# Performance work log

Measured on AMD Instinct MI355X. Metric: run time of the kernel, lower is better.

## Reference

```python
import jax, jax.numpy as jnp
import numpy as np

N_EMBD = 768
N_HEAD = 12
B, T = 4, 2048
EPS = 1e-5


def layernorm(x, w, b):
    mu = jnp.mean(x, axis=-1, keepdims=True)
    var = jnp.mean(jnp.square(x - mu), axis=-1, keepdims=True)
    return (x - mu) * jax.lax.rsqrt(var + EPS) * w + b


def setup_inputs() -> dict:
    key = jax.random.key(0)
    ks = jax.random.split(key, 6)
    C = N_EMBD
    s = 0.02
    return {
        "x": jax.random.normal(ks[0], (B, T, C), jnp.float32),
        "ln1_w": jnp.ones((C,), jnp.float32),
        "ln1_b": jnp.zeros((C,), jnp.float32),
        "W_qkv": jax.random.normal(ks[1], (C, 3 * C), jnp.float32) * s,
        "b_qkv": jnp.zeros((3 * C,), jnp.float32),
        "W_attnproj": jax.random.normal(ks[2], (C, C), jnp.float32) * s,
        "b_attnproj": jnp.zeros((C,), jnp.float32),
        "ln2_w": jnp.ones((C,), jnp.float32),
        "ln2_b": jnp.zeros((C,), jnp.float32),
        "W_fc": jax.random.normal(ks[3], (C, 4 * C), jnp.float32) * s,
        "b_fc": jnp.zeros((4 * C,), jnp.float32),
        "W_mlpproj": jax.random.normal(ks[4], (4 * C, C), jnp.float32) * s,
        "b_mlpproj": jnp.zeros((C,), jnp.float32),
    }


def reference(x, ln1_w, ln1_b, W_qkv, b_qkv, W_attnproj, b_attnproj,
              ln2_w, ln2_b, W_fc, b_fc, W_mlpproj, b_mlpproj):
    Bx, Tx, C = x.shape
    H = N_HEAD
    Dh = C // H

    # --- attention branch ---
    h = layernorm(x, ln1_w, ln1_b)
    qkv = h @ W_qkv + b_qkv                       # [B, T, 3C]
    q, k, v = jnp.split(qkv, 3, axis=-1)
    q = q.reshape(Bx, Tx, H, Dh).transpose(0, 2, 1, 3)  # [B, H, T, Dh]
    k = k.reshape(Bx, Tx, H, Dh).transpose(0, 2, 1, 3)
    v = v.reshape(Bx, Tx, H, Dh).transpose(0, 2, 1, 3)
    att = jnp.einsum('bhqd,bhkd->bhqk', q, k) * (1.0 / np.sqrt(Dh))
    att = jax.nn.softmax(att, axis=-1)            # full softmax attention (no mask)
    y = jnp.einsum('bhqk,bhkd->bhqd', att, v)     # [B, H, T, Dh]
    y = y.transpose(0, 2, 1, 3).reshape(Bx, Tx, C)
    y = y @ W_attnproj + b_attnproj
    x = x + y

    # --- MLP branch ---
    h = layernorm(x, ln2_w, ln2_b)
    h = jax.nn.gelu(h @ W_fc + b_fc, approximate=False)
    h = h @ W_mlpproj + b_mlpproj
    return x + h
```

## Files before the change

### kernel.cpp

```cpp
#include <hip/hip_runtime.h>

typedef __bf16 bf16x8 __attribute__((ext_vector_type(8)));
typedef __bf16 bf16x4 __attribute__((ext_vector_type(4)));
typedef float f32x4 __attribute__((ext_vector_type(4)));
typedef unsigned short u16;
typedef unsigned long long u64;

#define GL2LDS(gp, lp) __builtin_amdgcn_global_load_lds(                      \
    (const __attribute__((address_space(1))) void*)(gp),                      \
    (__attribute__((address_space(3))) void*)(lp), 16, 0, 0)

__device__ __forceinline__ u16 f2u(float f) {
    __bf16 h = (__bf16)f;
    return __builtin_bit_cast(u16, h);
}

__device__ __forceinline__ float fexp2(float x) {
    float r;
    asm("v_exp_f32 %0, %1" : "=v"(r) : "v"(x));
    return r;
}

__device__ __forceinline__ float frcp(float x) {
    float r;
    asm("v_rcp_f32 %0, %1" : "=v"(r) : "v"(x));
    return r;
}

__device__ __forceinline__ float gelu(float x) {
    const float a = x * x;
    const float b = fmaf(a, 0.10294323f, 2.30220795f);
    const float u = fexp2(x * b);
    const float r = frcp(1.0f + u);
    return (x > 8.0f) ? x : x * u * r;
}

template <int N>
__device__ __forceinline__ void waitv() {
    if constexpr (N == 0) asm volatile("s_waitcnt vmcnt(0)" ::: "memory");
    else if constexpr (N == 3) asm volatile("s_waitcnt vmcnt(3)" ::: "memory");
    else if constexpr (N == 4) asm volatile("s_waitcnt vmcnt(4)" ::: "memory");
    else if constexpr (N == 6) asm volatile("s_waitcnt vmcnt(6)" ::: "memory");
    else if constexpr (N == 8) asm volatile("s_waitcnt vmcnt(8)" ::: "memory");
}

__device__ __forceinline__ f32x4 mfma16(bf16x8 a, bf16x8 b, f32x4 c) {
    return __builtin_amdgcn_mfma_f32_16x16x32_bf16(a, b, c, 0, 0, 0);
}

__global__ __launch_bounds__(256) void transpose_kernel(
    const float* __restrict__ W, u16* __restrict__ Wt, int K, int N) {
    __shared__ float tile[32][33];
    const int tx = threadIdx.x & 31, ty = threadIdx.x >> 5;
    const int n0 = blockIdx.x * 32, k0 = blockIdx.y * 32;
#pragma unroll
    for (int i = 0; i < 4; i++)
        tile[ty + 8 * i][tx] = W[(size_t)(k0 + ty + 8 * i) * N + n0 + tx];
    __syncthreads();
#pragma unroll
    for (int i = 0; i < 4; i++)
        Wt[(size_t)(n0 + ty + 8 * i) * K + k0 + tx] = f2u(tile[tx][ty + 8 * i]);
}

__global__ __launch_bounds__(256) void ln_kernel(
    const float* __restrict__ xin, const float* __restrict__ wgt,
    const float* __restrict__ bia, u16* __restrict__ outp) {
    const int row = blockIdx.x, t = threadIdx.x;
    const float* xr = xin + (size_t)row * 768;
    float v0 = xr[t], v1 = xr[t + 256], v2 = xr[t + 512];
    float s = v0 + v1 + v2;
    float ss = v0 * v0 + v1 * v1 + v2 * v2;
#pragma unroll
    for (int off = 32; off; off >>= 1) {
        s += __shfl_xor(s, off);
        ss += __shfl_xor(ss, off);
    }
    __shared__ float red[8];
    const int w = t >> 6;
    if ((t & 63) == 0) { red[w] = s; red[4 + w] = ss; }
    __syncthreads();
    s  = red[0] + red[1] + red[2] + red[3];
    ss = red[4] + red[5] + red[6] + red[7];
    const float mu = s * (1.f / 768.f);
    const float var = ss * (1.f / 768.f) - mu * mu;
    const float rs = rsqrtf(var + 1e-5f);
    u16* orow = outp + (size_t)row * 768;
    orow[t]       = f2u((v0 - mu) * rs * wgt[t]       + bia[t]);
    orow[t + 256] = f2u((v1 - mu) * rs * wgt[t + 256] + bia[t + 256]);
    orow[t + 512] = f2u((v2 - mu) * rs * wgt[t + 512] + bia[t + 512]);
}

template <int BM, int BN, int DEPTH, int EPI>
__global__ __launch_bounds__(256, 3) void gemm_bt(
    const u16* __restrict__ A, const u16* __restrict__ Bt,
    const float* __restrict__ bias, const float* __restrict__ res,
    void* __restrict__ outp, u16* __restrict__ vt, int M, int N, int K) {
    constexpr int MM = BM / 32;
    constexpr int NN = BN / 32;
    constexpr int L = BM / 64 + BN / 64;
    constexpr int NBUF = DEPTH + 1;
    __shared__ __align__(16) u16 As[NBUF][BM * 32];
    __shared__ __align__(16) u16 Bs[NBUF][BN * 32];
    const int t = threadIdx.x;
    const int lane = t & 63, w = t >> 6;
    const int wg0 = blockIdx.y * gridDim.x + blockIdx.x;
    const int xcd = wg0 & 7, loc = wg0 >> 3;
    const int gx = gridDim.x, gy = gridDim.y;
    const int m0 = (xcd * (gy >> 3) + loc / gx) * BM;
    const int n0 = (loc % gx) * BN;
    const int wm = (w >> 1) * (BM / 2), wn = (w & 1) * (BN / 2);
    const int lq = lane & 15, g = lane >> 4;

    f32x4 acc[MM][NN];
#pragma unroll
    for (int i = 0; i < MM; i++)
#pragma unroll
        for (int j = 0; j < NN; j++) acc[i][j] = (f32x4){0.f, 0.f, 0.f, 0.f};

    const int srow = t >> 2;
    const int scl = (t & 3) ^ ((t >> 3) & 3);
    const u16* gA0 = A + (size_t)(m0 + srow) * K + scl * 8;
    const u16* gA1 = A + (size_t)(m0 + 64 + srow) * K + scl * 8;
    const u16* gB0 = Bt + (size_t)(n0 + srow) * K + scl * 8;
    const u16* gB1 = Bt + (size_t)(n0 + 64 + srow) * K + scl * 8;

    const int cph = g ^ ((lq >> 1) & 3);
    const int KT = K >> 5;

#define STAGE(buf, kt)                                                        \
    do {                                                                      \
        const int k0_ = (kt) << 5;                                            \
        char* lA_ = (char*)As[buf] + w * 1024;                                \
        char* lB_ = (char*)Bs[buf] + w * 1024;                                \
        GL2LDS(gA0 + k0_, lA_);                                               \
        if (BM == 128) GL2LDS(gA1 + k0_, lA_ + 4096);                         \
        GL2LDS(gB0 + k0_, lB_);                                               \
        if (BN == 128) GL2LDS(gB1 + k0_, lB_ + 4096);                         \
    } while (0)

#pragma unroll
    for (int d = 0; d < DEPTH; d++) STAGE(d, d);
    int cur = 0;
    for (int kt = 0; kt < KT; ++kt) {
        const int ahead = KT - 1 - kt;
        if (ahead >= DEPTH - 1) waitv<(DEPTH - 1) * L>();
        else if (DEPTH == 3 && ahead == 1) waitv<L>();
        else waitv<0>();
        __builtin_amdgcn_s_barrier();
        __builtin_amdgcn_sched_barrier(0);
        const char* rA = (char*)As[cur] + (wm + lq) * 64 + cph * 16;
        const char* rB = (char*)Bs[cur] + (wn + lq) * 64 + cph * 16;
        bf16x8 af[MM], bfr[NN];
#pragma unroll
        for (int m = 0; m < MM; m++) af[m] = *(const bf16x8*)(rA + m * 1024);
#pragma unroll
        for (int n = 0; n < NN; n++) bfr[n] = *(const bf16x8*)(rB + n * 1024);
#pragma unroll
        for (int m = 0; m < MM; m++)
#pragma unroll
            for (int n = 0; n < NN; n++)
                acc[m][n] = mfma16(af[m], bfr[n], acc[m][n]);
        if (kt + DEPTH < KT) {
            int nb = cur + DEPTH;
            if (nb >= NBUF) nb -= NBUF;
            STAGE(nb, kt + DEPTH);
        }
        cur = (cur == NBUF - 1) ? 0 : cur + 1;
    }
#undef STAGE

#pragma unroll
    for (int n = 0; n < NN; n++) {
        const int col = n0 + wn + 16 * n + lq;
        const float bv = bias[col];
#pragma unroll
        for (int m = 0; m < MM; m++) {
            const int rbase = m0 + wm + 16 * m + 4 * g;
            if constexpr (EPI == 0) {
                if (col < 1536) {
                    const float sc = (col < 768) ? 0.18033688f : 1.0f;
#pragma unroll
                    for (int r = 0; r < 4; r++) {
                        const size_t idx = (size_t)(rbase + r) * N + col;
                        ((u16*)outp)[idx] = f2u((acc[m][n][r] + bv) * sc);
                    }
                } else {
                    const int d = col - 1536;
                    bf16x4 pk;
#pragma unroll
                    for (int r = 0; r < 4; r++)
                        pk[r] = (__bf16)(acc[m][n][r] + bv);
                    u16* vrow = vt +
                        ((size_t)((rbase >> 11) * 12 + (d >> 6)) * 64 + (d & 63)) * 2048 +
                        (rbase & 2047);
                    *(u64*)vrow = __builtin_bit_cast(u64, pk);
                }
            } else {
#pragma unroll
                for (int r = 0; r < 4; r++) {
                    const size_t idx = (size_t)(rbase + r) * N + col;
                    const float v = acc[m][n][r] + bv;
                    if constexpr (EPI == 1) {
                        ((float*)outp)[idx] = v + res[idx];
                    } else {
                        ((u16*)outp)[idx] = f2u(gelu(v));
                    }
                }
            }
        }
    }
}

__global__ __launch_bounds__(256, 3) void attn_kernel(
    const u16* __restrict__ qkv, const u16* __restrict__ Vt,
    u16* __restrict__ y) {
    __shared__ __align__(16) u16 Ks[2][4096];
    __shared__ __align__(16) u16 Vts[2][4096];
    __shared__ __align__(16) u16 Ps[4][2048];
    const int t = threadIdx.x, lane = t & 63, w = t >> 6;
    int wg = blockIdx.y * gridDim.x + blockIdx.x;
    wg = (wg & 7) * ((gridDim.x * gridDim.y) >> 3) + (wg >> 3);
    const int bh = wg / gridDim.x;
    const int b = bh / 12, h = bh % 12;
    const int q0 = (wg % gridDim.x) * 128 + w * 32;
    const int lq = lane & 15, g = lane >> 4;
    const int swz = (lq & 7) << 4;

    bf16x8 qf[2][2];
#pragma unroll
    for (int qh = 0; qh < 2; qh++) {
        const u16* qp =
            qkv + (size_t)(b * 2048 + q0 + qh * 16 + lq) * 2304 + h * 64 + g * 8;
        qf[qh][0] = *(const bf16x8*)(qp);
        qf[qh][1] = *(const bf16x8*)(qp + 32);
    }
    bf16x8 ones;
#pragma unroll
    for (int i = 0; i < 8; i++) ones[i] = (__bf16)1.0f;

    f32x4 acc_o[2][4], acc_s[2];
#pragma unroll
    for (int qh = 0; qh < 2; qh++) {
        acc_s[qh] = (f32x4){0.f, 0.f, 0.f, 0.f};
#pragma unroll
        for (int f = 0; f < 4; f++) acc_o[qh][f] = (f32x4){0.f, 0.f, 0.f, 0.f};
    }

    const int srow = t >> 3, sc = (t & 7) ^ (srow & 7);
    const u16* kg = qkv + 768 + h * 64 + sc * 8 + (size_t)(b * 2048 + srow) * 2304;
    const u16* vg = Vt + (size_t)(bh * 64 + srow) * 2048 + sc * 8;

    int cur = 0;
    GL2LDS(kg, (char*)Ks[0] + w * 1024);
    GL2LDS(kg + (size_t)32 * 2304, (char*)Ks[0] + w * 1024 + 4096);
    GL2LDS(vg, (char*)Vts[0] + w * 1024);
    GL2LDS(vg + 32 * 2048, (char*)Vts[0] + w * 1024 + 4096);
    __syncthreads();

    for (int k0 = 0; k0 < 2048; k0 += 64) {
        if (k0 + 64 < 2048) {
            const int kn = k0 + 64;
            GL2LDS(kg + (size_t)kn * 2304, (char*)Ks[cur ^ 1] + w * 1024);
            GL2LDS(kg + (size_t)(kn + 32) * 2304,
                   (char*)Ks[cur ^ 1] + w * 1024 + 4096);
            GL2LDS(vg + kn, (char*)Vts[cur ^ 1] + w * 1024);
            GL2LDS(vg + 32 * 2048 + kn, (char*)Vts[cur ^ 1] + w * 1024 + 4096);
        }
        const char* KB = (const char*)Ks[cur];
        const char* VB = (const char*)Vts[cur];

        f32x4 st[2][4];
        __builtin_amdgcn_s_setprio(1);
#pragma unroll
        for (int kb = 0; kb < 4; kb++) {
            st[0][kb] = (f32x4){0.f, 0.f, 0.f, 0.f};
            st[1][kb] = (f32x4){0.f, 0.f, 0.f, 0.f};
            const char* kr = KB + (kb * 16 + lq) * 128;
#pragma unroll
            for (int dh = 0; dh < 2; dh++) {
                const bf16x8 kf =
                    *(const bf16x8*)(kr + ((((dh << 2) + g) << 4) ^ swz));
                st[0][kb] = mfma16(kf, qf[0][dh], st[0][kb]);
                st[1][kb] = mfma16(kf, qf[1][dh], st[1][kb]);
            }
        }
        __builtin_amdgcn_s_setprio(0);

#pragma unroll
        for (int qh = 0; qh < 2; qh++) {
            char* pw = (char*)Ps[w] + (qh * 16 + lq) * 128 + ((g & 1) << 3);
#pragma unroll
            for (int kb = 0; kb < 4; kb++) {
                bf16x4 pb;
#pragma unroll
                for (int r = 0; r < 4; r++)
                    pb[r] = (__bf16)fexp2(st[qh][kb][r]);
                *(u64*)(pw + ((((kb << 1) + (g >> 1)) << 4) ^ swz)) =
                    __builtin_bit_cast(u64, pb);
            }
        }

        __builtin_amdgcn_s_setprio(1);
#pragma unroll
        for (int kk = 0; kk < 2; kk++) {
            const int co = ((kk << 2) + g) << 4;
            bf16x8 vf[4];
#pragma unroll
            for (int f = 0; f < 4; f++)
                vf[f] = *(const bf16x8*)(VB + (16 * f + lq) * 128 + (co ^ swz));
#pragma unroll
            for (int qh = 0; qh < 2; qh++) {
                const bf16x8 pf = *(const bf16x8*)(
                    (const char*)Ps[w] + (qh * 16 + lq) * 128 + (co ^ swz));
#pragma unroll
                for (int f = 0; f < 4; f++)
                    acc_o[qh][f] = mfma16(vf[f], pf, acc_o[qh][f]);
                acc_s[qh] = mfma16(ones, pf, acc_s[qh]);
            }
        }
        __builtin_amdgcn_s_setprio(0);
        __syncthreads();
        cur ^= 1;
    }

#pragma unroll
    for (int qh = 0; qh < 2; qh++) {
        const float rinv = frcp(acc_s[qh][0]);
        char* yb = (char*)(y + (size_t)(b * 2048 + q0 + qh * 16 + lq) * 768 +
                           h * 64);
#pragma unroll
        for (int f = 0; f < 4; f++) {
            bf16x4 pk;
#pragma unroll
            for (int r = 0; r < 4; r++) pk[r] = (__bf16)(acc_o[qh][f][r] * rinv);
            *(u64*)(yb + f * 32 + g * 8) = __builtin_bit_cast(u64, pk);
        }
    }
}

extern "C" void kernel_launch(void* const* d_in, const int* in_sizes, int n_in,
                              void* d_out, int out_size, void* d_ws,
                              size_t ws_size, hipStream_t stream) {
    const float* x    = (const float*)d_in[0];
    const float* ln1w = (const float*)d_in[1];
    const float* ln1b = (const float*)d_in[2];
    const float* Wqkv = (const float*)d_in[3];
    const float* bqkv = (const float*)d_in[4];
    const float* Wap  = (const float*)d_in[5];
    const float* bap  = (const float*)d_in[6];
    const float* ln2w = (const float*)d_in[7];
    const float* ln2b = (const float*)d_in[8];
    const float* Wfc  = (const float*)d_in[9];
    const float* bfc  = (const float*)d_in[10];
    const float* Wmp  = (const float*)d_in[11];
    const float* bmp  = (const float*)d_in[12];
    float* out = (float*)d_out;

    char* ws = (char*)d_ws;
    u16* Wt_qkv = (u16*)(ws);
    u16* Wt_ap  = (u16*)(ws + 3538944);
    u16* Wt_fc  = (u16*)(ws + 4718592);
    u16* Wt_mp  = (u16*)(ws + 9437184);
    u16* bufA   = (u16*)(ws + 14155776);
    u16* bufB   = (u16*)(ws + 26738688);
    u16* VtBuf  = (u16*)(ws + 64487424);

    transpose_kernel<<<dim3(72, 24), 256, 0, stream>>>(Wqkv, Wt_qkv, 768, 2304);
    transpose_kernel<<<dim3(24, 24), 256, 0, stream>>>(Wap, Wt_ap, 768, 768);
    transpose_kernel<<<dim3(96, 24), 256, 0, stream>>>(Wfc, Wt_fc, 768, 3072);
    transpose_kernel<<<dim3(24, 96), 256, 0, stream>>>(Wmp, Wt_mp, 3072, 768);

    ln_kernel<<<8192, 256, 0, stream>>>(x, ln1w, ln1b, bufA);
    gemm_bt<128, 128, 2, 0><<<dim3(18, 64), 256, 0, stream>>>(
        bufA, Wt_qkv, bqkv, nullptr, bufB, VtBuf, 8192, 2304, 768);
    attn_kernel<<<dim3(16, 48), 256, 0, stream>>>(bufB, VtBuf, bufA);
    gemm_bt<64, 128, 3, 1><<<dim3(6, 128), 256, 0, stream>>>(
        bufA, Wt_ap, bap, x, out, nullptr, 8192, 768, 768);
    ln_kernel<<<8192, 256, 0, stream>>>(out, ln2w, ln2b, bufA);
    gemm_bt<128, 128, 2, 2><<<dim3(24, 64), 256, 0, stream>>>(
        bufA, Wt_fc, bfc, nullptr, bufB, nullptr, 8192, 3072, 768);
    gemm_bt<64, 128, 3, 1><<<dim3(6, 128), 256, 0, stream>>>(
        bufB, Wt_mp, bmp, out, out, nullptr, 8192, 768, 3072);
}
```

Before: 285.6 us.

## Replace GEMMs with 8-wave 128x256 tile kernel using split-K-half double buffering

Replaces the templated 256-thread GEMM with a 512-thread kernel that computes a 128x256 output tile per block, with each wave owning a 64x64 sub-tile. The K loop now steps by 64 and is double-buffered in two halves, each with its own barrier, and MFMA sections are wrapped in s_setprio. The larger tile is meant to raise operand reuse per LDS byte and improve MFMA density. The cost is fewer blocks for the N=768 projections (192 blocks), which may underfill the GPU, and more LDS per block.

```diff
diff --git a/kernel.cpp b/kernel.cpp
--- a/kernel.cpp
+++ b/kernel.cpp
@@ -39,9 +39,6 @@
 __device__ __forceinline__ void waitv() {
     if constexpr (N == 0) asm volatile("s_waitcnt vmcnt(0)" ::: "memory");
     else if constexpr (N == 3) asm volatile("s_waitcnt vmcnt(3)" ::: "memory");
-    else if constexpr (N == 4) asm volatile("s_waitcnt vmcnt(4)" ::: "memory");
-    else if constexpr (N == 6) asm volatile("s_waitcnt vmcnt(6)" ::: "memory");
-    else if constexpr (N == 8) asm volatile("s_waitcnt vmcnt(8)" ::: "memory");
 }
 
 __device__ __forceinline__ f32x4 mfma16(bf16x8 a, bf16x8 b, f32x4 c) {
@@ -90,91 +87,92 @@
     orow[t + 512] = f2u((v2 - mu) * rs * wgt[t + 512] + bia[t + 512]);
 }
 
-template <int BM, int BN, int DEPTH, int EPI>
-__global__ __launch_bounds__(256, 3) void gemm_bt(
+template <int EPI>
+__global__ __launch_bounds__(512, 2) void gemm8(
     const u16* __restrict__ A, const u16* __restrict__ Bt,
     const float* __restrict__ bias, const float* __restrict__ res,
     void* __restrict__ outp, u16* __restrict__ vt, int M, int N, int K) {
-    constexpr int MM = BM / 32;
-    constexpr int NN = BN / 32;
-    constexpr int L = BM / 64 + BN / 64;
-    constexpr int NBUF = DEPTH + 1;
-    __shared__ __align__(16) u16 As[NBUF][BM * 32];
-    __shared__ __align__(16) u16 Bs[NBUF][BN * 32];
+    __shared__ __align__(16) u16 As[16384];
+    __shared__ __align__(16) u16 Bs[32768];
     const int t = threadIdx.x;
     const int lane = t & 63, w = t >> 6;
     const int wg0 = blockIdx.y * gridDim.x + blockIdx.x;
     const int xcd = wg0 & 7, loc = wg0 >> 3;
-    const int gx = gridDim.x, gy = gridDim.y;
-    const int m0 = (xcd * (gy >> 3) + loc / gx) * BM;
-    const int n0 = (loc % gx) * BN;
-    const int wm = (w >> 1) * (BM / 2), wn = (w & 1) * (BN / 2);
+    const int gx = gridDim.x;
+    const int m0 = (xcd * 8 + loc / gx) * 128;
+    const int n0 = (loc % gx) * 256;
+    const int wm = (w >> 2) * 64, wn = (w & 3) * 64;
     const int lq = lane & 15, g = lane >> 4;
 
-    f32x4 acc[MM][NN];
-#pragma unroll
-    for (int i = 0; i < MM; i++)
-#pragma unroll
-        for (int j = 0; j < NN; j++) acc[i][j] = (f32x4){0.f, 0.f, 0.f, 0.f};
-
-    const int srow = t >> 2;
-    const int scl = (t & 3) ^ ((t >> 3) & 3);
-    const u16* gA0 = A + (size_t)(m0 + srow) * K + scl * 8;
-    const u16* gA1 = A + (size_t)(m0 + 64 + srow) * K + scl * 8;
-    const u16* gB0 = Bt + (size_t)(n0 + srow) * K + scl * 8;
-    const u16* gB1 = Bt + (size_t)(n0 + 64 + srow) * K + scl * 8;
-
-    const int cph = g ^ ((lq >> 1) & 3);
-    const int KT = K >> 5;
-
-#define STAGE(buf, kt)                                                        \
+    f32x4 acc[4][4];
+#pragma unroll
+    for (int i = 0; i < 4; i++)
+#pragma unroll
+        for (int j = 0; j < 4; j++) acc[i][j] = (f32x4){0.f, 0.f, 0.f, 0.f};
+
+    const int cl0 = 4 * ((lane >> 2) & 1) + ((lane & 3) ^ ((lane >> 3) & 3));
+    const int ka0 = cl0 * 8, ka1 = (cl0 ^ 4) * 8;
+    const u16* gA  = A  + (size_t)(m0 + w * 16 + (lane >> 2)) * K;
+    const u16* gB0 = Bt + (size_t)(n0 + w * 32 + (lane >> 2)) * K;
+    const u16* gB1 = Bt + (size_t)(n0 + w * 32 + 16 + (lane >> 2)) * K;
+
+    const int lsw = (g ^ ((lq >> 1) & 3)) << 4;
+    const int hpar = lq & 1;
+
+#define STAGE(buf, kt, h)                                                     \
     do {                                                                      \
-        const int k0_ = (kt) << 5;                                            \
-        char* lA_ = (char*)As[buf] + w * 1024;                                \
-        char* lB_ = (char*)Bs[buf] + w * 1024;                                \
-        GL2LDS(gA0 + k0_, lA_);                                               \
-        if (BM == 128) GL2LDS(gA1 + k0_, lA_ + 4096);                         \
-        GL2LDS(gB0 + k0_, lB_);                                               \
-        if (BN == 128) GL2LDS(gB1 + k0_, lB_ + 4096);                         \
+        const int ko_ = (kt) * 64 + ((h) ? ka1 : ka0);                        \
+        GL2LDS(gA + ko_, (char*)As + (buf) * 16384 + (h) * 8192 + w * 1024);  \
+        GL2LDS(gB0 + ko_, (char*)Bs + (buf) * 32768 + (h) * 16384 + w * 2048);\
+        GL2LDS(gB1 + ko_,                                                     \
+               (char*)Bs + (buf) * 32768 + (h) * 16384 + w * 2048 + 1024);    \
     } while (0)
 
-#pragma unroll
-    for (int d = 0; d < DEPTH; d++) STAGE(d, d);
-    int cur = 0;
+#define PHASE(buf, s)                                                         \
+    do {                                                                      \
+        const char* aB_ = (char*)As + (buf) * 16384 +                         \
+                          (((s) ^ hpar) ? 8192 : 0) + (wm + lq) * 64 + lsw;   \
+        const char* bB_ = (char*)Bs + (buf) * 32768 +                         \
+                          (((s) ^ hpar) ? 16384 : 0) + (wn + lq) * 64 + lsw;  \
+        bf16x8 af[4], bfr[4];                                                 \
+        _Pragma("unroll")                                                     \
+        for (int m = 0; m < 4; m++) af[m] = *(const bf16x8*)(aB_ + m * 1024); \
+        _Pragma("unroll")                                                     \
+        for (int n = 0; n < 4; n++) bfr[n] = *(const bf16x8*)(bB_ + n * 1024);\
+        __builtin_amdgcn_s_setprio(1);                                        \
+        _Pragma("unroll")                                                     \
+        for (int m = 0; m < 4; m++)                                           \
+            _Pragma("unroll")                                                 \
+            for (int n = 0; n < 4; n++)                                       \
+                acc[m][n] = mfma16(af[m], bfr[n], acc[m][n]);                 \
+        __builtin_amdgcn_s_setprio(0);                                        \
+    } while (0)
+
+    const int KT = K >> 6;
+    STAGE(0, 0, 0);
+    STAGE(0, 0, 1);
     for (int kt = 0; kt < KT; ++kt) {
-        const int ahead = KT - 1 - kt;
-        if (ahead >= DEPTH - 1) waitv<(DEPTH - 1) * L>();
-        else if (DEPTH == 3 && ahead == 1) waitv<L>();
-        else waitv<0>();
+        const int buf = kt & 1;
+        waitv<3>();
         __builtin_amdgcn_s_barrier();
         __builtin_amdgcn_sched_barrier(0);
-        const char* rA = (char*)As[cur] + (wm + lq) * 64 + cph * 16;
-        const char* rB = (char*)Bs[cur] + (wn + lq) * 64 + cph * 16;
-        bf16x8 af[MM], bfr[NN];
-#pragma unroll
-        for (int m = 0; m < MM; m++) af[m] = *(const bf16x8*)(rA + m * 1024);
-#pragma unroll
-        for (int n = 0; n < NN; n++) bfr[n] = *(const bf16x8*)(rB + n * 1024);
-#pragma unroll
-        for (int m = 0; m < MM; m++)
-#pragma unroll
-            for (int n = 0; n < NN; n++)
-                acc[m][n] = mfma16(af[m], bfr[n], acc[m][n]);
-        if (kt + DEPTH < KT) {
-            int nb = cur + DEPTH;
-            if (nb >= NBUF) nb -= NBUF;
-            STAGE(nb, kt + DEPTH);
-        }
-        cur = (cur == NBUF - 1) ? 0 : cur + 1;
+        if (kt + 1 < KT) STAGE(buf ^ 1, kt + 1, 0);
+        PHASE(buf, 0);
+        if (kt + 1 < KT) waitv<3>(); else waitv<0>();
+        __builtin_amdgcn_s_barrier();
+        __builtin_amdgcn_sched_barrier(0);
+        if (kt + 1 < KT) STAGE(buf ^ 1, kt + 1, 1);
+        PHASE(buf, 1);
     }
 #undef STAGE
-
-#pragma unroll
-    for (int n = 0; n < NN; n++) {
+#undef PHASE
+
+#pragma unroll
+    for (int n = 0; n < 4; n++) {
         const int col = n0 + wn + 16 * n + lq;
         const float bv = bias[col];
 #pragma unroll
-        for (int m = 0; m < MM; m++) {
+        for (int m = 0; m < 4; m++) {
             const int rbase = m0 + wm + 16 * m + 4 * g;
             if constexpr (EPI == 0) {
                 if (col < 1536) {
@@ -371,14 +369,14 @@
     transpose_kernel<<<dim3(24, 96), 256, 0, stream>>>(Wmp, Wt_mp, 3072, 768);
 
     ln_kernel<<<8192, 256, 0, stream>>>(x, ln1w, ln1b, bufA);
-    gemm_bt<128, 128, 2, 0><<<dim3(18, 64), 256, 0, stream>>>(
+    gemm8<0><<<dim3(9, 64), 512, 0, stream>>>(
         bufA, Wt_qkv, bqkv, nullptr, bufB, VtBuf, 8192, 2304, 768);
     attn_kernel<<<dim3(16, 48), 256, 0, stream>>>(bufB, VtBuf, bufA);
-    gemm_bt<64, 128, 3, 1><<<dim3(6, 128), 256, 0, stream>>>(
+    gemm8<1><<<dim3(3, 64), 512, 0, stream>>>(
         bufA, Wt_ap, bap, x, out, nullptr, 8192, 768, 768);
     ln_kernel<<<8192, 256, 0, stream>>>(out, ln2w, ln2b, bufA);
-    gemm_bt<128, 128, 2, 2><<<dim3(24, 64), 256, 0, stream>>>(
+    gemm8<2><<<dim3(12, 64), 512, 0, stream>>>(
         bufA, Wt_fc, bfc, nullptr, bufB, nullptr, 8192, 3072, 768);
-    gemm_bt<64, 128, 3, 1><<<dim3(6, 128), 256, 0, stream>>>(
+    gemm8<1><<<dim3(3, 64), 512, 0, stream>>>(
         bufB, Wt_mp, bmp, out, out, nullptr, 8192, 768, 3072);
 }
```

Result: slower. 340.4 us (+19.2%).
